# Kernel optimization log

Measured on AMD Instinct MI355X. Metric: run time of the kernel, lower is better.

## Reference

```python
import jax, jax.numpy as jnp
import numpy as np

# dims
B, T = 2, 256
E = 512            # n_embd
G = 8              # n_groups
GD = E // G        # group_dim == head_dim == 64
L = 8              # n_layer
N = L * G          # n_nodes == 64
V = 50257          # vocab
S = 8              # n_steps


def _rms(x):
    eps = jnp.asarray(jnp.finfo(x.dtype).eps, x.dtype)
    return x * jax.lax.rsqrt(jnp.mean(x * x, axis=-1, keepdims=True) + eps)


def _rope(x, cos, sin):
    # x: (B,T,N,GD); cos/sin: (T, GD//2)
    d = x.shape[-1] // 2
    x1, x2 = x[..., :d], x[..., d:]
    c = cos[None, :, None, :]
    s = sin[None, :, None, :]
    return jnp.concatenate([x1 * c + x2 * s, -x1 * s + x2 * c], axis=-1)


def setup_inputs() -> dict:
    key = jax.random.key(0)
    ks = jax.random.split(key, 9)
    idx = jax.random.randint(ks[0], (B, T), 0, V, dtype=jnp.int32)
    wte = 0.02 * jax.random.normal(ks[1], (V, E), jnp.float32)
    # adapters: identity block at group slice (per init_weights) + small noise
    ad = np.zeros((N, GD, E), np.float32)
    for i in range(N):
        g = i % G
        ad[i, :, g * GD:(g + 1) * GD] = np.eye(GD, dtype=np.float32)
    adapters = jnp.asarray(ad) + 0.005 * jax.random.normal(ks[2], (N, GD, E), jnp.float32)
    qkv_w = 0.005 * jax.random.normal(ks[3], (N, 3 * GD, GD), jnp.float32)
    attn_proj = 0.005 * jax.random.normal(ks[4], (N, GD, GD), jnp.float32)
    mlp_fc = 0.005 * jax.random.normal(ks[5], (N, 4 * GD, GD), jnp.float32)
    mlp_proj = 0.005 * jax.random.normal(ks[6], (N, GD, 4 * GD), jnp.float32)
    # structured dependency matrix: layer l <- layer l-1, weight 1/G
    D = np.zeros((N, N), np.float32)
    for l in range(1, L):
        D[l * G:(l + 1) * G, (l - 1) * G:l * G] = 1.0 / G
    dep = jnp.asarray(D)
    router_w = (1.0 / np.sqrt(E)) * jax.random.normal(ks[7], (E, 1), jnp.float32)
    router_b = jnp.full((1,), -3.0, jnp.float32)
    lm_head_w = 0.005 * jax.random.normal(ks[8], (V, E), jnp.float32)
    return {"idx": idx, "n_steps": S, "wte": wte, "adapters": adapters,
            "qkv_w": qkv_w, "attn_proj": attn_proj, "mlp_fc": mlp_fc,
            "mlp_proj": mlp_proj, "dep": dep, "router_w": router_w,
            "router_b": router_b, "lm_head_w": lm_head_w}


def _forward(idx, n_steps, wte, adapters, qkv_w, attn_proj, mlp_fc, mlp_proj,
             dep, router_w, router_b, lm_head_w):
    Bs, Ts = idx.shape
    groups = np.arange(N) % G  # static scatter/gather pattern: node -> group slice
    inv_freq = 1.0 / (10000.0 ** (np.arange(0, GD, 2, dtype=np.float64) / GD))
    freqs = np.outer(np.arange(Ts), inv_freq)
    cos = jnp.asarray(np.cos(freqs), jnp.float32)
    sin = jnp.asarray(np.sin(freqs), jnp.float32)

    x = _rms(wte[idx])                                  # (B,T,E)
    p_cont = jnp.ones((Bs, Ts), x.dtype)

    # depths computed under no_grad in torch -> stop_gradient here
    dp = jax.nn.relu(jax.lax.stop_gradient(dep))
    depths = jnp.zeros((N,), x.dtype)
    for _ in range(L):
        depths = dp @ (depths + 1.0)

    causal = np.tril(np.ones((Ts, Ts), bool))
    scale = 1.0 / np.sqrt(GD)

    for t in range(n_steps):
        td = t * (L / n_steps)
        w_all = jnp.exp(-jnp.abs(depths - td))
        # torch gathers active = w_all > 0.15; equivalent dense form: zero-weight inactive
        w_eff = jnp.where(w_all > 0.15, w_all, jnp.zeros_like(w_all))

        xi = (jnp.einsum('bte,nge->btng', x, adapters)
              + x.reshape(Bs, Ts, G, GD)[:, :, groups, :])          # (B,T,N,GD)
        qkv = jnp.einsum('btng,nog->btno', xi, qkv_w).reshape(Bs, Ts, N, 3, GD)
        q, k, v = qkv[..., 0, :], qkv[..., 1, :], qkv[..., 2, :]
        q = _rms(_rope(q, cos, sin))
        k = _rms(_rope(k, cos, sin))
        scores = jnp.einsum('btng,bsng->bnts', q, k) * scale
        scores = jnp.where(causal[None, None], scores, -jnp.inf)
        att = jnp.einsum('bnts,bsng->btng', jax.nn.softmax(scores, axis=-1), v)
        # NOTE: einsum strings below intentionally replicate the original code
        # (k and o are summed out without contraction against the other operand)
        xi_mid = xi + jnp.einsum('btng,ngk->btng', att, attn_proj)
        fc = jnp.einsum('btng,nog->btno', _rms(xi_mid), mlp_fc)
        mp = jnp.einsum('btno,ngk->btng', jnp.square(jax.nn.relu(fc)), mlp_proj)
        up = (xi_mid + mp - xi) * w_eff[None, None, :, None]
        # scatter-add back by group (node n = l*G + g -> group g)
        full_up = up.reshape(Bs, Ts, L, G, GD).sum(axis=2).reshape(Bs, Ts, E)
        x = x + full_up * p_cont[..., None]
        # router (training-mode soft halting; top_fixed=bottom_fixed=0)
        ph = jax.nn.sigmoid(x @ router_w + router_b)[..., 0]
        p_cont = p_cont * (1.0 - ph)

    logits = _rms(x) @ lm_head_w.T
    return 15.0 * jnp.tanh(logits / 15.0)


def reference(idx, n_steps, wte, adapters, qkv_w, attn_proj, mlp_fc, mlp_proj,
              dep, router_w, router_b, lm_head_w):
    return _forward(idx, n_steps, wte, adapters, qkv_w, attn_proj, mlp_fc,
                    mlp_proj, dep, router_w, router_b, lm_head_w)
```

## Files before the change

kernel.cpp:

```cpp
#include <hip/hip_runtime.h>
#include <hip/hip_bf16.h>
#include <math.h>

#define BB 2
#define TT 256
#define BT 512
#define EE 512
#define GG 8
#define GD 64
#define LL 8
#define NN 64
#define VV 50257
#define D2 32
#define EPS 1.1920928955078125e-07f
#define S72 72

typedef __attribute__((ext_vector_type(4))) float floatx4;
typedef __attribute__((ext_vector_type(8))) short short8;

#define OFF_DEPTHS   0
#define OFF_APS      64
#define OFF_MPS      (OFF_APS + NN*GD)
#define OFF_COS      (OFF_MPS + NN*GD)
#define OFF_SIN      (OFF_COS + TT*D2)
#define OFF_X        (OFF_SIN + TT*D2)
#define OFF_PCONT    (OFF_X + BT*EE)
#define OFF_SMLP     (OFF_PCONT + BT)
#define OFF_YBF      (OFF_SMLP + BT*NN)
#define OFF_STEP     (OFF_YBF + (BT*EE)/2)
#define OFF_XI       OFF_STEP
#define OFF_ATT      (OFF_XI + BT*NN*GD)
#define OFF_XBF      (OFF_ATT + BT*NN*GD)
#define OFF_QB       (OFF_XBF + (BT*EE)/2)
#define OFF_KB       (OFF_QB + (BT*NN*GD)/2)
#define OFF_VTB      (OFF_KB + (BT*NN*GD)/2)
#define OFF_ABF      (OFF_VTB + (BT*NN*GD)/2)
#define OFF_QWBF     (OFF_ABF + (NN*GD*EE)/2)
#define OFF_FWBF     (OFF_QWBF + (NN*192*GD)/2)
#define OFF_WBF      OFF_STEP

__device__ __forceinline__ float step_weight(const float* depths, const int* ns, int t, int n) {
    float td = (float)t * (8.0f / (float)ns[0]);
    float wa = expf(-fabsf(depths[n] - td));
    return (wa > 0.15f) ? wa : 0.0f;
}

__global__ void k_prep(const float* __restrict__ dep, float* __restrict__ depths) {
    __shared__ float cur[NN], nxt[NN];
    int i = threadIdx.x;
    if (i < NN) cur[i] = 0.f;
    __syncthreads();
    for (int it = 0; it < LL; ++it) {
        if (i < NN) {
            float acc = 0.f;
            for (int m = 0; m < NN; ++m) acc += fmaxf(dep[i*NN + m], 0.f) * (cur[m] + 1.f);
            nxt[i] = acc;
        }
        __syncthreads();
        if (i < NN) cur[i] = nxt[i];
        __syncthreads();
    }
    if (i < NN) depths[i] = cur[i];
}

__global__ void k_sums(const float* __restrict__ attn_proj, const float* __restrict__ mlp_proj,
                       float* __restrict__ aps, float* __restrict__ mps) {
    int i = blockIdx.x * blockDim.x + threadIdx.x;
    if (i >= NN*GD) return;
    float a = 0.f;
    const float* ap = attn_proj + (size_t)i * GD;
    for (int k = 0; k < GD; ++k) a += ap[k];
    aps[i] = a;
    float m = 0.f;
    const float* mp = mlp_proj + (size_t)i * 4 * GD;
    for (int k = 0; k < 4*GD; ++k) m += mp[k];
    mps[i] = m;
}

__global__ void k_rope_table(float* __restrict__ ctab, float* __restrict__ stab) {
    int i = blockIdx.x * blockDim.x + threadIdx.x;
    if (i >= TT*D2) return;
    int pos = i / D2, f = i % D2;
    double inv = pow(10000.0, -((double)(2*f)) / (double)GD);
    double ang = (double)pos * inv;
    ctab[i] = (float)cos(ang);
    stab[i] = (float)sin(ang);
}

__global__ void k_cvt(const float* __restrict__ src, __hip_bfloat16* __restrict__ dst, int n4) {
    int i = blockIdx.x * blockDim.x + threadIdx.x;
    if (i >= n4) return;
    float4 f = ((const float4*)src)[i];
    __hip_bfloat16 h0 = __float2bfloat16(f.x);
    __hip_bfloat16 h1 = __float2bfloat16(f.y);
    __hip_bfloat16 h2 = __float2bfloat16(f.z);
    __hip_bfloat16 h3 = __float2bfloat16(f.w);
    ushort4 o;
    o.x = *(const unsigned short*)&h0;
    o.y = *(const unsigned short*)&h1;
    o.z = *(const unsigned short*)&h2;
    o.w = *(const unsigned short*)&h3;
    *(ushort4*)(dst + (size_t)i*4) = o;
}

__global__ void k_embed(const int* __restrict__ idx, const float* __restrict__ wte,
                        float* __restrict__ x, __hip_bfloat16* __restrict__ xbf,
                        float* __restrict__ pcont) {
    int bt = blockIdx.x;
    int tid = threadIdx.x;
    const float* src = wte + (size_t)idx[bt] * EE;
    float v0 = src[tid], v1 = src[tid + 256];
    __shared__ float red[4];
    float ss = v0*v0 + v1*v1;
    for (int o = 32; o > 0; o >>= 1) ss += __shfl_xor(ss, o);
    if ((tid & 63) == 0) red[tid >> 6] = ss;
    __syncthreads();
    float sc = rsqrtf((red[0]+red[1]+red[2]+red[3]) / (float)EE + EPS);
    float a = v0 * sc, b = v1 * sc;
    x[bt*EE + tid]       = a;
    x[bt*EE + tid + 256] = b;
    xbf[bt*EE + tid]       = __float2bfloat16(a);
    xbf[bt*EE + tid + 256] = __float2bfloat16(b);
    if (tid == 0) pcont[bt] = 1.f;
}

__global__ __launch_bounds__(256) void k_xi_qkv(const __hip_bfloat16* __restrict__ xbf,
        const __hip_bfloat16* __restrict__ abf, const __hip_bfloat16* __restrict__ qwbf,
        const float* __restrict__ x, float* __restrict__ xi,
        __hip_bfloat16* __restrict__ qb, __hip_bfloat16* __restrict__ kb,
        __hip_bfloat16* __restrict__ vtb,
        const float* __restrict__ ctab, const float* __restrict__ stab,
        const float* __restrict__ depths, const int* __restrict__ ns, int t) {
    int n = blockIdx.y;
    if (step_weight(depths, ns, t, n) == 0.f) return;
    int bt0 = blockIdx.x * 64;
    __shared__ __align__(16) char smem[64*65*4 + 64*S72*2 + 64*S72*2];
    __hip_bfloat16* As  = (__hip_bfloat16*)smem;
    float*          obuf = (float*)smem;
    __hip_bfloat16* Bs  = (__hip_bfloat16*)(smem + 64*65*4);
    __hip_bfloat16* xis = (__hip_bfloat16*)(smem + 64*65*4 + 64*S72*2);
    int tid = threadIdx.x;
    int wave = tid >> 6, lane = tid & 63;
    int wr = wave >> 1, wc = wave & 1;
    int quad = lane >> 4, l16 = lane & 15;

    floatx4 acc[2][2];
    #pragma unroll
    for (int mt = 0; mt < 2; ++mt)
        #pragma unroll
        for (int nt = 0; nt < 2; ++nt) acc[mt][nt] = (floatx4){0.f,0.f,0.f,0.f};
    for (int k0 = 0; k0 < EE; k0 += 64) {
        for (int i = tid; i < 512; i += 256) {
            int r = i >> 3, c8 = (i & 7) * 8;
            *(uint4*)(&As[r*S72 + c8]) = *(const uint4*)(&xbf[(size_t)(bt0 + r)*EE + k0 + c8]);
            *(uint4*)(&Bs[r*S72 + c8]) = *(const uint4*)(&abf[((size_t)n*GD + r)*EE + k0 + c8]);
        }
        __syncthreads();
        #pragma unroll
        for (int ks = 0; ks < 2; ++ks) {
            short8 af[2], bf[2];
            #pragma unroll
            for (int mt = 0; mt < 2; ++mt)
                af[mt] = *(const short8*)(&As[(wr*32 + mt*16 + l16)*S72 + ks*32 + quad*8]);
            #pragma unroll
            for (int nt = 0; nt < 2; ++nt)
                bf[nt] = *(const short8*)(&Bs[(wc*32 + nt*16 + l16)*S72 + ks*32 + quad*8]);
            #pragma unroll
            for (int mt = 0; mt < 2; ++mt)
                #pragma unroll
                for (int nt = 0; nt < 2; ++nt)
                    acc[mt][nt] = __builtin_amdgcn_mfma_f32_16x16x32_bf16(af[mt], bf[nt], acc[mt][nt], 0, 0, 0);
        }
        __syncthreads();
    }
    int gofs = (n & (GG-1)) * GD;
    #pragma unroll
    for (int mt = 0; mt < 2; ++mt) {
        #pragma unroll
        for (int nt = 0; nt < 2; ++nt) {
            int col = wc*32 + nt*16 + l16;
            #pragma unroll
            for (int r = 0; r < 4; ++r) {
                int token = wr*32 + mt*16 + quad*4 + r;
                int bt = bt0 + token;
                float val = acc[mt][nt][r] + x[(size_t)bt*EE + gofs + col];
                xi[((size_t)bt*NN + n)*GD + col] = val;
                xis[token*S72 + col] = __float2bfloat16(val);
            }
        }
    }
    __syncthreads();

    const __hip_bfloat16* wbase = qwbf + (size_t)n * 192 * GD;
    int b = bt0 >> 8;
    int t0 = bt0 & (TT - 1);
    for (int c = 0; c < 3; ++c) {
        for (int i = tid; i < 512; i += 256) {
            int r = i >> 3, c8 = (i & 7) * 8;
            *(uint4*)(&Bs[r*S72 + c8]) = *(const uint4*)(&wbase[(size_t)(c*64 + r)*GD + c8]);
        }
        __syncthreads();
        floatx4 oacc[2][2];
        #pragma unroll
        for (int mt = 0; mt < 2; ++mt)
            #pragma unroll
            for (int nt = 0; nt < 2; ++nt) oacc[mt][nt] = (floatx4){0.f,0.f,0.f,0.f};
        #pragma unroll
        for (int ks = 0; ks < 2; ++ks) {
            short8 af[2], bf[2];
            #pragma unroll
            for (int mt = 0; mt < 2; ++mt)
                af[mt] = *(const short8*)(&xis[(wr*32 + mt*16 + l16)*S72 + ks*32 + quad*8]);
            #pragma unroll
            for (int nt = 0; nt < 2; ++nt)
                bf[nt] = *(const short8*)(&Bs[(wc*32 + nt*16 + l16)*S72 + ks*32 + quad*8]);
            #pragma unroll
            for (int mt = 0; mt < 2; ++mt)
                #pragma unroll
                for (int nt = 0; nt < 2; ++nt)
                    oacc[mt][nt] = __builtin_amdgcn_mfma_f32_16x16x32_bf16(af[mt], bf[nt], oacc[mt][nt], 0, 0, 0);
        }
        #pragma unroll
        for (int mt = 0; mt < 2; ++mt)
            #pragma unroll
            for (int nt = 0; nt < 2; ++nt)
                #pragma unroll
                for (int r = 0; r < 4; ++r)
                    obuf[(wr*32 + mt*16 + quad*4 + r)*65 + wc*32 + nt*16 + l16] = oacc[mt][nt][r];
        __syncthreads();
        if (c < 2) {
            __hip_bfloat16* dst = (c == 0) ? qb : kb;
            for (int tr = 0; tr < 16; ++tr) {
                int row = wave*16 + tr, bt = bt0 + row;
                float val = obuf[row*65 + lane];
                int pos = bt & (TT - 1);
                float pair = __shfl_xor(val, 32);
                int fi = lane & 31;
                float cc = ctab[pos*D2 + fi], sn = stab[pos*D2 + fi];
                float nv = (lane < 32) ? (val*cc + pair*sn) : (val*cc - pair*sn);
                float ss = nv*nv;
                for (int o = 32; o > 0; o >>= 1) ss += __shfl_xor(ss, o);
                float outv = nv * rsqrtf(ss / (float)GD + EPS);
                dst[((size_t)bt*NN + n)*GD + lane] = __float2bfloat16(outv);
            }
        } else {
            for (int tr = 0; tr < 16; ++tr) {
                int g = wave*16 + tr;
                float vv = obuf[lane*65 + g];
                vtb[(((size_t)(b*NN + n))*GD + g)*TT + t0 + lane] = __float2bfloat16(vv);
            }
        }
        __syncthreads();
    }
}

__global__ __launch_bounds__(256) void k_attn(const __hip_bfloat16* __restrict__ qb,
        const __hip_bfloat16* __restrict__ kb, const __hip_bfloat16* __restrict__ vtb,
        float* __restrict__ att,
        const float* __restrict__ depths, const int* __restrict__ ns, int t) {
    int it = blockIdx.x, b = blockIdx.y, n = blockIdx.z;
    if (step_weight(depths, ns, t, n) == 0.f) return;
    __shared__ __align__(16) __hip_bfloat16 qs[64*S72];
    __shared__ __align__(16) __hip_bfloat16 ksm[64*S72];
    __shared__ __align__(16) __hip_bfloat16 vs[64*S72];
    __shared__ __align__(16) __hip_bfloat16 ps[64*S72];
    int tid = threadIdx.x;
    int wave = tid >> 6, lane = tid & 63;
    int quad = lane >> 4, l16 = lane & 15;
    for (int i = tid; i < 512; i += 256) {
        int r = i >> 3, c8 = (i & 7) * 8;
        *(uint4*)(&qs[r*S72 + c8]) = *(const uint4*)(&qb[(((size_t)(b*TT + it*64 + r))*NN + n)*GD + c8]);
    }
    floatx4 oacc[4];
    float m_i[4], l_i[4];
    #pragma unroll
    for (int nt = 0; nt < 4; ++nt) oacc[nt] = (floatx4){0.f,0.f,0.f,0.f};
    #pragma unroll
    for (int r = 0; r < 4; ++r) { m_i[r] = -INFINITY; l_i[r] = 0.f; }
    __syncthreads();
    for (int ct = 0; ct <= it; ++ct) {
        for (int i = tid; i < 512; i += 256) {
            int r = i >> 3, c8 = (i & 7) * 8;
            *(uint4*)(&ksm[r*S72 + c8]) = *(const uint4*)(&kb[(((size_t)(b*TT + ct*64 + r))*NN + n)*GD + c8]);
            *(uint4*)(&vs[r*S72 + c8])  = *(const uint4*)(&vtb[(((size_t)(b*NN + n))*GD + r)*TT + ct*64 + c8]);
        }
        __syncthreads();
        floatx4 s[4];
        #pragma unroll
        for (int nt = 0; nt < 4; ++nt) s[nt] = (floatx4){0.f,0.f,0.f,0.f};
        #pragma unroll
        for (int ks = 0; ks < 2; ++ks) {
            short8 af = *(const short8*)(&qs[(wave*16 + l16)*S72 + ks*32 + quad*8]);
            #pragma unroll
            for (int nt = 0; nt < 4; ++nt) {
                short8 bf = *(const short8*)(&ksm[(nt*16 + l16)*S72 + ks*32 + quad*8]);
                s[nt] = __builtin_amdgcn_mfma_f32_16x16x32_bf16(af, bf, s[nt], 0, 0, 0);
            }
        }
        #pragma unroll
        for (int r = 0; r < 4; ++r) {
            int rowg = it*64 + wave*16 + quad*4 + r;
            float mx = -INFINITY;
            #pragma unroll
            for (int nt = 0; nt < 4; ++nt) {
                int colg = ct*64 + nt*16 + l16;
                float sv = (colg <= rowg) ? s[nt][r] * 0.125f : -INFINITY;
                s[nt][r] = sv;
                mx = fmaxf(mx, sv);
            }
            for (int o = 8; o > 0; o >>= 1) mx = fmaxf(mx, __shfl_xor(mx, o));
            float mnew = fmaxf(m_i[r], mx);
            float alpha = expf(m_i[r] - mnew);
            float rs = 0.f;
            #pragma unroll
            for (int nt = 0; nt < 4; ++nt) {
                float p = expf(s[nt][r] - mnew);
                s[nt][r] = p;
                rs += p;
            }
            for (int o = 8; o > 0; o >>= 1) rs += __shfl_xor(rs, o);
            l_i[r] = l_i[r]*alpha + rs;
            m_i[r] = mnew;
            #pragma unroll
            for (int nt = 0; nt < 4; ++nt) oacc[nt][r] *= alpha;
        }
        #pragma unroll
        for (int nt = 0; nt < 4; ++nt)
            #pragma unroll
            for (int r = 0; r < 4; ++r)
                ps[(wave*16 + quad*4 + r)*S72 + nt*16 + l16] = __float2bfloat16(s[nt][r]);
        __syncthreads();
        #pragma unroll
        for (int ks = 0; ks < 2; ++ks) {
            short8 af = *(const short8*)(&ps[(wave*16 + l16)*S72 + ks*32 + quad*8]);
            #pragma unroll
            for (int nt = 0; nt < 4; ++nt) {
                short8 bf = *(const short8*)(&vs[(nt*16 + l16)*S72 + ks*32 + quad*8]);
                oacc[nt] = __builtin_amdgcn_mfma_f32_16x16x32_bf16(af, bf, oacc[nt], 0, 0, 0);
            }
        }
        __syncthreads();
    }
    #pragma unroll
    for (int r = 0; r < 4; ++r) {
        float inv = 1.f / l_i[r];
        int token = it*64 + wave*16 + quad*4 + r;
        #pragma unroll
        for (int nt = 0; nt < 4; ++nt)
            att[((size_t)(b*TT + token)*NN + n)*GD + nt*16 + l16] = oacc[nt][r] * inv;
    }
}

__global__ __launch_bounds__(256) void k_fc2(const float* __restrict__ xi, const float* __restrict__ att,
        const float* __restrict__ aps, const __hip_bfloat16* __restrict__ fwbf, float* __restrict__ smlp,
        const float* __restrict__ depths, const int* __restrict__ ns, int t) {
    int n = blockIdx.y;
    if (step_weight(depths, ns, t, n) == 0.f) return;
    int bt0 = blockIdx.x * 64;
    __shared__ __align__(16) __hip_bfloat16 ys[64*S72];
    __shared__ __align__(16) __hip_bfloat16 ws[64*S72];
    __shared__ float sred[64];
    int tid = threadIdx.x;
    int wave = tid >> 6, lane = tid & 63;
    int quad = lane >> 4, l16 = lane & 15;
    for (int tr = 0; tr < 16; ++tr) {
        int row = wave*16 + tr, bt = bt0 + row;
        size_t base = ((size_t)bt*NN + n)*GD + lane;
        float xv = xi[base] + att[base] * aps[n*GD + lane];
        float ss = xv*xv;
        for (int o = 32; o > 0; o >>= 1) ss += __shfl_xor(ss, o);
        ys[row*S72 + lane] = __float2bfloat16(xv * rsqrtf(ss / (float)GD + EPS));
    }
    __syncthreads();
    float rowacc[4] = {0.f, 0.f, 0.f, 0.f};
    for (int c = 0; c < 4; ++c) {
        for (int i = tid; i < 512; i += 256) {
            int r = i >> 3, c8 = (i & 7) * 8;
            *(uint4*)(&ws[r*S72 + c8]) = *(const uint4*)(&fwbf[((size_t)n*256 + c*64 + r)*GD + c8]);
        }
        __syncthreads();
        floatx4 s[4];
        #pragma unroll
        for (int nt = 0; nt < 4; ++nt) s[nt] = (floatx4){0.f,0.f,0.f,0.f};
        #pragma unroll
        for (int ks = 0; ks < 2; ++ks) {
            short8 af = *(const short8*)(&ys[(wave*16 + l16)*S72 + ks*32 + quad*8]);
            #pragma unroll
            for (int nt = 0; nt < 4; ++nt) {
                short8 bf = *(const short8*)(&ws[(nt*16 + l16)*S72 + ks*32 + quad*8]);
                s[nt] = __builtin_amdgcn_mfma_f32_16x16x32_bf16(af, bf, s[nt], 0, 0, 0);
            }
        }
        #pragma unroll
        for (int nt = 0; nt < 4; ++nt)
            #pragma unroll
            for (int r = 0; r < 4; ++r) {
                float rr = fmaxf(s[nt][r], 0.f);
                rowacc[r] += rr*rr;
            }
        __syncthreads();
    }
    #pragma unroll
    for (int r = 0; r < 4; ++r) {
        for (int o = 8; o > 0; o >>= 1) rowacc[r] += __shfl_xor(rowacc[r], o);
        if (l16 == 0) sred[wave*16 + quad*4 + r] = rowacc[r];
    }
    __syncthreads();
    if (tid < 64) smlp[(size_t)(bt0 + tid)*NN + n] = sred[tid];
}

__global__ __launch_bounds__(256) void k_update(float* __restrict__ x, __hip_bfloat16* __restrict__ xbf,
                                                float* __restrict__ pcont,
                                                const float* __restrict__ att, const float* __restrict__ smlp,
                                                const float* __restrict__ aps, const float* __restrict__ mps,
                                                const float* __restrict__ router_w, const float* __restrict__ router_b,
                                                const float* __restrict__ depths, const int* __restrict__ ns, int t,
                                                int last, __hip_bfloat16* __restrict__ ybf) {
    int bt = blockIdx.x, tid = threadIdx.x;
    __shared__ float we[NN];
    __shared__ float red[4];
    __shared__ float red2[4];
    if (tid < NN) we[tid] = step_weight(depths, ns, t, tid);
    __syncthreads();
    float pc = pcont[bt];
    float dot = 0.f, ssq = 0.f;
    float xv0 = 0.f, xv1 = 0.f;
    #pragma unroll
    for (int h = 0; h < 2; ++h) {
        int e = tid + h*256;
        int gq = e >> 6, gd = e & 63;
        float sum = 0.f;
        #pragma unroll
        for (int l = 0; l < LL; ++l) {
            int n = l*GG + gq;
            float w = we[n];
            if (w != 0.f) {
                sum += (att[((size_t)bt*NN + n)*GD + gd] * aps[n*GD + gd]
                        + smlp[bt*NN + n] * mps[n*GD + gd]) * w;
            }
        }
        float xv = x[bt*EE + e] + sum * pc;
        x[bt*EE + e] = xv;
        if (!last) xbf[bt*EE + e] = __float2bfloat16(xv);
        dot += xv * router_w[e];
        ssq += xv * xv;
        if (h == 0) xv0 = xv; else xv1 = xv;
    }
    for (int o = 32; o > 0; o >>= 1) dot += __shfl_xor(dot, o);
    if (last) for (int o = 32; o > 0; o >>= 1) ssq += __shfl_xor(ssq, o);
    if ((tid & 63) == 0) { red[tid >> 6] = dot; red2[tid >> 6] = ssq; }
    __syncthreads();
    if (last) {
        float sc = rsqrtf((red2[0]+red2[1]+red2[2]+red2[3]) / (float)EE + EPS);
        ybf[bt*EE + tid]       = __float2bfloat16(xv0 * sc);
        ybf[bt*EE + tid + 256] = __float2bfloat16(xv1 * sc);
    }
    if (tid == 0) {
        float z = red[0]+red[1]+red[2]+red[3] + router_b[0];
        float ph = 1.f / (1.f + expf(-z));
        pcont[bt] = pc * (1.f - ph);
    }
}

__global__ __launch_bounds__(256) void k_lmhead(const __hip_bfloat16* __restrict__ ybf,
                                                const __hip_bfloat16* __restrict__ wbf,
                                                float* __restrict__ out) {
    int id = blockIdx.x;
    int bnLow = id & 7;
    int rest = id >> 3;
    int bm = rest & 3;
    int bnHigh = rest >> 2;
    int bn = bnHigh*8 + bnLow;
    if (bn >= (VV + 127)/128) return;

    __shared__ __align__(16) __hip_bfloat16 As[128*64];
    __shared__ __align__(16) __hip_bfloat16 Bs[128*64];
    int tid = threadIdx.x;
    int wave = tid >> 6, lane = tid & 63;
    int wr = wave >> 1, wc = wave & 1;
    int quad = lane >> 4, l16 = lane & 15;

    size_t offA[4], offB[4];
    int ldsOff[4];
    #pragma unroll
    for (int j = 0; j < 4; ++j) {
        int s = (j*4 + wave)*64 + lane;
        int r = s >> 3;
        int cs = (s & 7) ^ (r & 7);
        offA[j] = (size_t)(bm*128 + r)*EE + cs*8;
        int vrow = bn*128 + r; if (vrow >= VV) vrow = VV - 1;
        offB[j] = (size_t)vrow*EE + cs*8;
        ldsOff[j] = (j*4 + wave)*512;
    }

    floatx4 acc[4][4];
    #pragma unroll
    for (int mt = 0; mt < 4; ++mt)
        #pragma unroll
        for (int nt = 0; nt < 4; ++nt)
            acc[mt][nt] = (floatx4){0.f, 0.f, 0.f, 0.f};

    for (int k0 = 0; k0 < EE; k0 += 64) {
        #pragma unroll
        for (int j = 0; j < 4; ++j) {
            __builtin_amdgcn_global_load_lds(
                (const __attribute__((address_space(1))) void*)(ybf + offA[j] + k0),
                (__attribute__((address_space(3))) void*)(&As[ldsOff[j]]), 16, 0, 0);
            __builtin_amdgcn_global_load_lds(
                (const __attribute__((address_space(1))) void*)(wbf + offB[j] + k0),
                (__attribute__((address_space(3))) void*)(&Bs[ldsOff[j]]), 16, 0, 0);
        }
        __syncthreads();
        #pragma unroll
        for (int ks = 0; ks < 2; ++ks) {
            short8 af[4], bf[4];
            #pragma unroll
            for (int mt = 0; mt < 4; ++mt) {
                int r = wr*64 + mt*16 + l16;
                int ck = ((ks << 2) | quad) ^ (r & 7);
                af[mt] = *(const short8*)(&As[r*64 + ck*8]);
            }
            #pragma unroll
            for (int nt = 0; nt < 4; ++nt) {
                int r = wc*64 + nt*16 + l16;
                int ck = ((ks << 2) | quad) ^ (r & 7);
                bf[nt] = *(const short8*)(&Bs[r*64 + ck*8]);
            }
            #pragma unroll
            for (int mt = 0; mt < 4; ++mt)
                #pragma unroll
                for (int nt = 0; nt < 4; ++nt)
                    acc[mt][nt] = __builtin_amdgcn_mfma_f32_16x16x32_bf16(af[mt], bf[nt], acc[mt][nt], 0, 0, 0);
        }
        __syncthreads();
    }
    #pragma unroll
    for (int mt = 0; mt < 4; ++mt) {
        int gm = bm*128 + wr*64 + mt*16 + quad*4;
        #pragma unroll
        for (int nt = 0; nt < 4; ++nt) {
            int gn = bn*128 + wc*64 + nt*16 + l16;
            if (gn < VV) {
                #pragma unroll
                for (int r = 0; r < 4; ++r) {
                    float lv = acc[mt][nt][r];
                    out[(size_t)(gm + r)*VV + gn] = 15.f * tanhf(lv * (1.f/15.f));
                }
            }
        }
    }
}

extern "C" void kernel_launch(void* const* d_in, const int* in_sizes, int n_in,
                              void* d_out, int out_size, void* d_ws, size_t ws_size,
                              hipStream_t stream) {
    (void)in_sizes; (void)n_in; (void)out_size; (void)ws_size;
    const int*   idx       = (const int*)d_in[0];
    const int*   nsteps    = (const int*)d_in[1];
    const float* wte       = (const float*)d_in[2];
    const float* adapters  = (const float*)d_in[3];
    const float* qkv_w     = (const float*)d_in[4];
    const float* attn_proj = (const float*)d_in[5];
    const float* mlp_fc    = (const float*)d_in[6];
    const float* mlp_proj  = (const float*)d_in[7];
    const float* dep       = (const float*)d_in[8];
    const float* router_w  = (const float*)d_in[9];
    const float* router_b  = (const float*)d_in[10];
    const float* lm_head   = (const float*)d_in[11];
    float* out = (float*)d_out;
    float* ws  = (float*)d_ws;

    float* depths = ws + OFF_DEPTHS;
    float* aps    = ws + OFF_APS;
    float* mps    = ws + OFF_MPS;
    float* ctab   = ws + OFF_COS;
    float* stab   = ws + OFF_SIN;
    float* x      = ws + OFF_X;
    float* pcont  = ws + OFF_PCONT;
    float* smlp   = ws + OFF_SMLP;
    float* xi     = ws + OFF_XI;
    float* att    = ws + OFF_ATT;
    __hip_bfloat16* xbf  = (__hip_bfloat16*)(ws + OFF_XBF);
    __hip_bfloat16* qb   = (__hip_bfloat16*)(ws + OFF_QB);
    __hip_bfloat16* kb   = (__hip_bfloat16*)(ws + OFF_KB);
    __hip_bfloat16* vtb  = (__hip_bfloat16*)(ws + OFF_VTB);
    __hip_bfloat16* abf  = (__hip_bfloat16*)(ws + OFF_ABF);
    __hip_bfloat16* qwbf = (__hip_bfloat16*)(ws + OFF_QWBF);
    __hip_bfloat16* fwbf = (__hip_bfloat16*)(ws + OFF_FWBF);
    __hip_bfloat16* wbf  = (__hip_bfloat16*)(ws + OFF_WBF);
    __hip_bfloat16* ybf  = (__hip_bfloat16*)(ws + OFF_YBF);

    k_prep<<<1, 64, 0, stream>>>(dep, depths);
    k_sums<<<(NN*GD + 255)/256, 256, 0, stream>>>(attn_proj, mlp_proj, aps, mps);
    k_rope_table<<<(TT*D2 + 255)/256, 256, 0, stream>>>(ctab, stab);
    k_cvt<<<(NN*GD*EE/4 + 255)/256, 256, 0, stream>>>(adapters, abf, NN*GD*EE/4);
    k_cvt<<<(NN*192*GD/4 + 255)/256, 256, 0, stream>>>(qkv_w, qwbf, NN*192*GD/4);
    k_cvt<<<(NN*256*GD/4 + 255)/256, 256, 0, stream>>>(mlp_fc, fwbf, NN*256*GD/4);
    k_embed<<<BT, 256, 0, stream>>>(idx, wte, x, xbf, pcont);

    for (int t = 0; t < 8; ++t) {
        k_xi_qkv<<<dim3(BT/64, NN), 256, 0, stream>>>(xbf, abf, qwbf, x, xi, qb, kb, vtb,
                                                      ctab, stab, depths, nsteps, t);
        k_attn<<<dim3(4, BB, NN), 256, 0, stream>>>(qb, kb, vtb, att, depths, nsteps, t);
        k_fc2<<<dim3(BT/64, NN), 256, 0, stream>>>(xi, att, aps, fwbf, smlp, depths, nsteps, t);
        k_update<<<BT, 256, 0, stream>>>(x, xbf, pcont, att, smlp, aps, mps,
                                         router_w, router_b, depths, nsteps, t,
                                         (t == 7) ? 1 : 0, ybf);
    }

    k_cvt<<<((VV*EE)/4 + 255)/256, 256, 0, stream>>>(lm_head, wbf, (VV*EE)/4);
    k_lmhead<<<1600, 256, 0, stream>>>(ybf, wbf, out);
}
```

Measured before the change: 798.5 us.

## Double-buffer LDS loads in xi_qkv and lmhead, remap tiles, use fast tanh

The adapter GEMM in k_xi_qkv moves to async global_load_lds with an XOR-swizzled layout and double buffering, so the next K tile is prefetched while MFMAs run. The LM-head kernel also gets double-buffered LDS tiles, which doubles its shared memory. It also gets a new block-to-tile mapping that interleaves blocks across the vocab. The tanh epilogue is replaced by an exp-based fast formula. This costs more LDS per block, which may lower occupancy, and slightly reduces tanh accuracy.

```diff
diff --git a/kernel.cpp b/kernel.cpp
--- a/kernel.cpp
+++ b/kernel.cpp
@@ -134,37 +134,76 @@
     int n = blockIdx.y;
     if (step_weight(depths, ns, t, n) == 0.f) return;
     int bt0 = blockIdx.x * 64;
-    __shared__ __align__(16) char smem[64*65*4 + 64*S72*2 + 64*S72*2];
-    __hip_bfloat16* As  = (__hip_bfloat16*)smem;
+    __shared__ __align__(16) char smem[16640 + 16384 + 9216];
+    __hip_bfloat16* sA   = (__hip_bfloat16*)smem;
     float*          obuf = (float*)smem;
-    __hip_bfloat16* Bs  = (__hip_bfloat16*)(smem + 64*65*4);
-    __hip_bfloat16* xis = (__hip_bfloat16*)(smem + 64*65*4 + 64*S72*2);
+    __hip_bfloat16* sB   = (__hip_bfloat16*)(smem + 16640);
+    __hip_bfloat16* Bs72 = (__hip_bfloat16*)(smem + 16640);
+    __hip_bfloat16* xis  = (__hip_bfloat16*)(smem + 33024);
     int tid = threadIdx.x;
     int wave = tid >> 6, lane = tid & 63;
     int wr = wave >> 1, wc = wave & 1;
     int quad = lane >> 4, l16 = lane & 15;
 
+    size_t goffA[2], goffB[2];
+    int sOff[2];
+    #pragma unroll
+    for (int j = 0; j < 2; ++j) {
+        int s = (j*4 + wave)*64 + lane;
+        int r = s >> 3;
+        int cs = (s & 7) ^ (r & 7);
+        goffA[j] = (size_t)(bt0 + r)*EE + cs*8;
+        goffB[j] = ((size_t)n*GD + r)*EE + cs*8;
+        sOff[j] = (j*4 + wave)*512;
+    }
+
     floatx4 acc[2][2];
     #pragma unroll
     for (int mt = 0; mt < 2; ++mt)
         #pragma unroll
         for (int nt = 0; nt < 2; ++nt) acc[mt][nt] = (floatx4){0.f,0.f,0.f,0.f};
-    for (int k0 = 0; k0 < EE; k0 += 64) {
-        for (int i = tid; i < 512; i += 256) {
-            int r = i >> 3, c8 = (i & 7) * 8;
-            *(uint4*)(&As[r*S72 + c8]) = *(const uint4*)(&xbf[(size_t)(bt0 + r)*EE + k0 + c8]);
-            *(uint4*)(&Bs[r*S72 + c8]) = *(const uint4*)(&abf[((size_t)n*GD + r)*EE + k0 + c8]);
-        }
-        __syncthreads();
+
+    #pragma unroll
+    for (int j = 0; j < 2; ++j) {
+        __builtin_amdgcn_global_load_lds(
+            (const __attribute__((address_space(1))) void*)(xbf + goffA[j]),
+            (__attribute__((address_space(3))) void*)(&sA[sOff[j]]), 16, 0, 0);
+        __builtin_amdgcn_global_load_lds(
+            (const __attribute__((address_space(1))) void*)(abf + goffB[j]),
+            (__attribute__((address_space(3))) void*)(&sB[sOff[j]]), 16, 0, 0);
+    }
+    __syncthreads();
+
+    int cur = 0;
+    #pragma unroll
+    for (int kt = 0; kt < 8; ++kt) {
+        if (kt < 7) {
+            int k0 = (kt + 1) * 64;
+            #pragma unroll
+            for (int j = 0; j < 2; ++j) {
+                __builtin_amdgcn_global_load_lds(
+                    (const __attribute__((address_space(1))) void*)(xbf + goffA[j] + k0),
+                    (__attribute__((address_space(3))) void*)(&sA[(cur^1)*4096 + sOff[j]]), 16, 0, 0);
+                __builtin_amdgcn_global_load_lds(
+                    (const __attribute__((address_space(1))) void*)(abf + goffB[j] + k0),
+                    (__attribute__((address_space(3))) void*)(&sB[(cur^1)*4096 + sOff[j]]), 16, 0, 0);
+            }
+        }
         #pragma unroll
         for (int ks = 0; ks < 2; ++ks) {
             short8 af[2], bf[2];
             #pragma unroll
-            for (int mt = 0; mt < 2; ++mt)
-                af[mt] = *(const short8*)(&As[(wr*32 + mt*16 + l16)*S72 + ks*32 + quad*8]);
-            #pragma unroll
-            for (int nt = 0; nt < 2; ++nt)
-                bf[nt] = *(const short8*)(&Bs[(wc*32 + nt*16 + l16)*S72 + ks*32 + quad*8]);
+            for (int mt = 0; mt < 2; ++mt) {
+                int row = wr*32 + mt*16 + l16;
+                int ck = ((ks << 2) | quad) ^ (row & 7);
+                af[mt] = *(const short8*)(&sA[cur*4096 + row*64 + ck*8]);
+            }
+            #pragma unroll
+            for (int nt = 0; nt < 2; ++nt) {
+                int row = wc*32 + nt*16 + l16;
+                int ck = ((ks << 2) | quad) ^ (row & 7);
+                bf[nt] = *(const short8*)(&sB[cur*4096 + row*64 + ck*8]);
+            }
             #pragma unroll
             for (int mt = 0; mt < 2; ++mt)
                 #pragma unroll
@@ -172,7 +211,9 @@
                     acc[mt][nt] = __builtin_amdgcn_mfma_f32_16x16x32_bf16(af[mt], bf[nt], acc[mt][nt], 0, 0, 0);
         }
         __syncthreads();
-    }
+        cur ^= 1;
+    }
+
     int gofs = (n & (GG-1)) * GD;
     #pragma unroll
     for (int mt = 0; mt < 2; ++mt) {
@@ -197,7 +238,7 @@
     for (int c = 0; c < 3; ++c) {
         for (int i = tid; i < 512; i += 256) {
             int r = i >> 3, c8 = (i & 7) * 8;
-            *(uint4*)(&Bs[r*S72 + c8]) = *(const uint4*)(&wbase[(size_t)(c*64 + r)*GD + c8]);
+            *(uint4*)(&Bs72[r*S72 + c8]) = *(const uint4*)(&wbase[(size_t)(c*64 + r)*GD + c8]);
         }
         __syncthreads();
         floatx4 oacc[2][2];
@@ -213,7 +254,7 @@
                 af[mt] = *(const short8*)(&xis[(wr*32 + mt*16 + l16)*S72 + ks*32 + quad*8]);
             #pragma unroll
             for (int nt = 0; nt < 2; ++nt)
-                bf[nt] = *(const short8*)(&Bs[(wc*32 + nt*16 + l16)*S72 + ks*32 + quad*8]);
+                bf[nt] = *(const short8*)(&Bs72[(wc*32 + nt*16 + l16)*S72 + ks*32 + quad*8]);
             #pragma unroll
             for (int mt = 0; mt < 2; ++mt)
                 #pragma unroll
@@ -466,15 +507,13 @@
                                                 const __hip_bfloat16* __restrict__ wbf,
                                                 float* __restrict__ out) {
     int id = blockIdx.x;
-    int bnLow = id & 7;
-    int rest = id >> 3;
-    int bm = rest & 3;
-    int bnHigh = rest >> 2;
-    int bn = bnHigh*8 + bnLow;
+    int w = (id & 7) * 200 + (id >> 3);
+    int bm = w & 3;
+    int bn = w >> 2;
     if (bn >= (VV + 127)/128) return;
 
-    __shared__ __align__(16) __hip_bfloat16 As[128*64];
-    __shared__ __align__(16) __hip_bfloat16 Bs[128*64];
+    __shared__ __align__(16) __hip_bfloat16 As[2][128*64];
+    __shared__ __align__(16) __hip_bfloat16 Bs[2][128*64];
     int tid = threadIdx.x;
     int wave = tid >> 6, lane = tid & 63;
     int wr = wave >> 1, wc = wave & 1;
@@ -500,17 +539,31 @@
         for (int nt = 0; nt < 4; ++nt)
             acc[mt][nt] = (floatx4){0.f, 0.f, 0.f, 0.f};
 
-    for (int k0 = 0; k0 < EE; k0 += 64) {
-        #pragma unroll
-        for (int j = 0; j < 4; ++j) {
-            __builtin_amdgcn_global_load_lds(
-                (const __attribute__((address_space(1))) void*)(ybf + offA[j] + k0),
-                (__attribute__((address_space(3))) void*)(&As[ldsOff[j]]), 16, 0, 0);
-            __builtin_amdgcn_global_load_lds(
-                (const __attribute__((address_space(1))) void*)(wbf + offB[j] + k0),
-                (__attribute__((address_space(3))) void*)(&Bs[ldsOff[j]]), 16, 0, 0);
-        }
-        __syncthreads();
+    #pragma unroll
+    for (int j = 0; j < 4; ++j) {
+        __builtin_amdgcn_global_load_lds(
+            (const __attribute__((address_space(1))) void*)(ybf + offA[j]),
+            (__attribute__((address_space(3))) void*)(&As[0][ldsOff[j]]), 16, 0, 0);
+        __builtin_amdgcn_global_load_lds(
+            (const __attribute__((address_space(1))) void*)(wbf + offB[j]),
+            (__attribute__((address_space(3))) void*)(&Bs[0][ldsOff[j]]), 16, 0, 0);
+    }
+    __syncthreads();
+
+    int cur = 0;
+    for (int kt = 0; kt < 8; ++kt) {
+        if (kt < 7) {
+            int k0 = (kt + 1) * 64;
+            #pragma unroll
+            for (int j = 0; j < 4; ++j) {
+                __builtin_amdgcn_global_load_lds(
+                    (const __attribute__((address_space(1))) void*)(ybf + offA[j] + k0),
+                    (__attribute__((address_space(3))) void*)(&As[cur^1][ldsOff[j]]), 16, 0, 0);
+                __builtin_amdgcn_global_load_lds(
+                    (const __attribute__((address_space(1))) void*)(wbf + offB[j] + k0),
+                    (__attribute__((address_space(3))) void*)(&Bs[cur^1][ldsOff[j]]), 16, 0, 0);
+            }
+        }
         #pragma unroll
         for (int ks = 0; ks < 2; ++ks) {
             short8 af[4], bf[4];
@@ -518,13 +571,13 @@
             for (int mt = 0; mt < 4; ++mt) {
                 int r = wr*64 + mt*16 + l16;
                 int ck = ((ks << 2) | quad) ^ (r & 7);
-                af[mt] = *(const short8*)(&As[r*64 + ck*8]);
+                af[mt] = *(const short8*)(&As[cur][r*64 + ck*8]);
             }
             #pragma unroll
             for (int nt = 0; nt < 4; ++nt) {
                 int r = wc*64 + nt*16 + l16;
                 int ck = ((ks << 2) | quad) ^ (r & 7);
-                bf[nt] = *(const short8*)(&Bs[r*64 + ck*8]);
+                bf[nt] = *(const short8*)(&Bs[cur][r*64 + ck*8]);
             }
             #pragma unroll
             for (int mt = 0; mt < 4; ++mt)
@@ -533,7 +586,9 @@
                     acc[mt][nt] = __builtin_amdgcn_mfma_f32_16x16x32_bf16(af[mt], bf[nt], acc[mt][nt], 0, 0, 0);
         }
         __syncthreads();
-    }
+        cur ^= 1;
+    }
+
     #pragma unroll
     for (int mt = 0; mt < 4; ++mt) {
         int gm = bm*128 + wr*64 + mt*16 + quad*4;
@@ -543,8 +598,10 @@
             if (gn < VV) {
                 #pragma unroll
                 for (int r = 0; r < 4; ++r) {
-                    float lv = acc[mt][nt][r];
-                    out[(size_t)(gm + r)*VV + gn] = 15.f * tanhf(lv * (1.f/15.f));
+                    float u = acc[mt][nt][r] * (1.f/15.f);
+                    float e = __expf(2.f * u);
+                    float th = 1.f - __fdividef(2.f, e + 1.f);
+                    out[(size_t)(gm + r)*VV + gn] = 15.f * th;
                 }
             }
         }
```

Result: faster. 709.4 us (-11.2%).
